# Kernel tuning notes

Hardware: AMD Instinct MI355X
Metric: run time of the kernel (lower is better)

Reference implementation:

```python
import jax, jax.numpy as jnp
import numpy as np

N = 100000      # nodes
E = 1600000     # edges (avg degree 16)
IN_DIM = 64
H = 4           # num_heads
D = 32          # out_dim per head
NEG_SLOPE = 0.1


def setup_inputs() -> dict:
    key = jax.random.key(0)
    k_x, k_src, k_dst, k_w, k_fc, k_al, k_ar = jax.random.split(key, 7)
    x = jax.random.normal(k_x, (N, IN_DIM), dtype=jnp.float32)
    src = jax.random.randint(k_src, (E,), 0, N, dtype=jnp.int32)
    dst = jax.random.randint(k_dst, (E,), 0, N, dtype=jnp.int32)
    w = jax.random.uniform(k_w, (E,), dtype=jnp.float32)
    # xavier-ish init for learned params
    W_fc = jax.random.normal(k_fc, (IN_DIM, H * D), dtype=jnp.float32) * (2.0 / (IN_DIM + H * D)) ** 0.5
    attn_l = jax.random.normal(k_al, (1, H, D), dtype=jnp.float32) * 0.1
    attn_r = jax.random.normal(k_ar, (1, H, D), dtype=jnp.float32) * 0.1
    vt = jnp.zeros((1,), dtype=jnp.float32)  # unused by forward (as in the source)
    return {"vt": vt, "x": x, "src": src, "dst": dst, "w": w,
            "W_fc": W_fc, "attn_l": attn_l, "attn_r": attn_r}


def reference(vt, x, src, dst, w, W_fc, attn_l, attn_r):
    # node projection: [N, H, D]
    feat = (x @ W_fc).reshape(-1, H, D)
    el = jnp.sum(feat * attn_l, axis=-1)  # [N, H]
    er = jnp.sum(feat * attn_r, axis=-1)  # [N, H]
    # per-edge logits: u_add_v then leaky_relu, scaled by edge weight w
    e = el[src] + er[dst]                                   # [E, H]
    e = jnp.where(e >= 0, e, NEG_SLOPE * e)                 # leaky_relu
    e = w[:, None] * e                                      # [E, H]
    # edge softmax grouped by destination node (numerically stable)
    m = jax.ops.segment_max(e, dst, num_segments=N)         # [N, H]
    ex = jnp.exp(e - m[dst])                                # [E, H]
    den = jax.ops.segment_sum(ex, dst, num_segments=N)      # [N, H]
    a = ex / den[dst]                                       # [E, H]
    # message passing: u_mul_e -> sum over incoming edges
    msg = feat[src] * a[:, :, None]                         # [E, H, D]
    out = jax.ops.segment_sum(msg, dst, num_segments=N)     # [N, H, D]
    return out
```

## Files before the change

### kernel.cpp

```cpp
#include <hip/hip_runtime.h>
#include <math.h>

#define IN_DIM 64
#define HH 4
#define CC 128
#define NEG_SLOPE 0.1f

typedef __attribute__((ext_vector_type(8))) short short8;
typedef __attribute__((ext_vector_type(4))) float f32x4;

__device__ __forceinline__ float leaky(float v) { return v >= 0.f ? v : NEG_SLOPE * v; }

__device__ __forceinline__ unsigned f2bf(float f) {
  unsigned u = __float_as_uint(f);
  unsigned r = u + 0x7FFFu + ((u >> 16) & 1u);
  return r >> 16;
}

__global__ void k_prepw(const float* __restrict__ W, unsigned* __restrict__ wt) {
  int tid = blockIdx.x * 256 + threadIdx.x;
  if (tid >= 128 * 32) return;
  int n = tid >> 5;
  int r = tid & 31;
  int b = r >> 2, h = r & 3;
  int k = b * 8 + h * 2;
  unsigned lo = f2bf(W[k * CC + n]);
  unsigned hi = f2bf(W[(k + 1) * CC + n]);
  wt[n * 32 + (b ^ (n & 7)) * 4 + h] = lo | (hi << 16);
}

__global__ __launch_bounds__(256) void k_project(
    const float* __restrict__ x, const unsigned* __restrict__ wt,
    const float* __restrict__ attn_l, const float* __restrict__ attn_r,
    unsigned char* __restrict__ featQ, float* __restrict__ scale,
    float* __restrict__ el, float* __restrict__ er, int N)
{
  __shared__ unsigned Wlds[4096];
  __shared__ float Al[CC], Ar[CC];
  int t = threadIdx.x;
  {
    const uint4* s = (const uint4*)wt;
    uint4* d = (uint4*)Wlds;
#pragma unroll
    for (int i = 0; i < 4; ++i) d[t + 256 * i] = s[t + 256 * i];
  }
  if (t < CC) { Al[t] = attn_l[t]; Ar[t] = attn_r[t]; }
  __syncthreads();

  int lane = t & 63;
  int l4 = lane >> 4, l16 = lane & 15;
  int node = blockIdx.x * 64 + (t >> 6) * 16 + l16;
  bool valid = node < N;
  int nrow = valid ? node : 0;

  short8 bfr[2];
#pragma unroll
  for (int s = 0; s < 2; ++s) {
    const float4* xp = (const float4*)&x[(size_t)nrow * 64 + s * 32 + l4 * 8];
    float4 xa = xp[0], xb = xp[1];
    union { short8 v; unsigned u[4]; } pk;
    pk.u[0] = f2bf(xa.x) | (f2bf(xa.y) << 16);
    pk.u[1] = f2bf(xa.z) | (f2bf(xa.w) << 16);
    pk.u[2] = f2bf(xb.x) | (f2bf(xb.y) << 16);
    pk.u[3] = f2bf(xb.z) | (f2bf(xb.w) << 16);
    bfr[s] = pk.v;
  }

  f32x4 acc[8];
#pragma unroll
  for (int c = 0; c < 8; ++c) acc[c] = (f32x4){0.f, 0.f, 0.f, 0.f};

#pragma unroll
  for (int c = 0; c < 8; ++c) {
    int n0 = c * 16 + l16;
    int sw = n0 & 7;
#pragma unroll
    for (int s = 0; s < 2; ++s) {
      int b = s * 4 + l4;
      union { short8 v; uint4 q; } af;
      af.q = *(const uint4*)&Wlds[n0 * 32 + (b ^ sw) * 4];
      acc[c] = __builtin_amdgcn_mfma_f32_16x16x32_bf16(af.v, bfr[s], acc[c], 0, 0, 0);
    }
  }

  float mx = 0.f;
#pragma unroll
  for (int c = 0; c < 8; ++c) {
#pragma unroll
    for (int r = 0; r < 4; ++r) mx = fmaxf(mx, fabsf(acc[c][r]));
  }
  mx = fmaxf(mx, __shfl_xor(mx, 16, 64));
  mx = fmaxf(mx, __shfl_xor(mx, 32, 64));
  float mxs = fmaxf(mx, 1e-20f);
  float inv = 127.f / mxs;

  if (valid) {
#pragma unroll
    for (int c = 0; c < 8; ++c) {
      int q0 = __float2int_rn(acc[c][0] * inv) + 128;
      int q1 = __float2int_rn(acc[c][1] * inv) + 128;
      int q2 = __float2int_rn(acc[c][2] * inv) + 128;
      int q3 = __float2int_rn(acc[c][3] * inv) + 128;
      unsigned u = (unsigned)(q0 & 0xff) | ((unsigned)(q1 & 0xff) << 8) |
                   ((unsigned)(q2 & 0xff) << 16) | ((unsigned)(q3 & 0xff) << 24);
      *(unsigned*)&featQ[(size_t)node * 128 + c * 16 + l4 * 4] = u;
    }
    if (l4 == 0) scale[node] = mxs * (1.f / 127.f);
  }

  float pl[4], pr[4];
#pragma unroll
  for (int h = 0; h < 4; ++h) {
    float sl = 0.f, sr = 0.f;
#pragma unroll
    for (int ct = 0; ct < 2; ++ct) {
      int c = 2 * h + ct;
      int cb = c * 16 + l4 * 4;
#pragma unroll
      for (int r = 0; r < 4; ++r) {
        sl = fmaf(acc[c][r], Al[cb + r], sl);
        sr = fmaf(acc[c][r], Ar[cb + r], sr);
      }
    }
    sl += __shfl_xor(sl, 16, 64); sl += __shfl_xor(sl, 32, 64);
    sr += __shfl_xor(sr, 16, 64); sr += __shfl_xor(sr, 32, 64);
    pl[h] = sl; pr[h] = sr;
  }
  if (l4 == 0 && valid) {
    *(float4*)&el[(size_t)node * 4] = make_float4(pl[0], pl[1], pl[2], pl[3]);
    *(float4*)&er[(size_t)node * 4] = make_float4(pr[0], pr[1], pr[2], pr[3]);
  }
}

__global__ __launch_bounds__(256) void k_bhist(const int* __restrict__ dst,
                                               int* __restrict__ bcnt, int E, int NB) {
  __shared__ int lh[512];
  for (int i = threadIdx.x; i < NB; i += 256) lh[i] = 0;
  __syncthreads();
  int stride = gridDim.x * 256;
  for (int i = blockIdx.x * 256 + threadIdx.x; i < E; i += stride)
    atomicAdd(&lh[dst[i] >> 8], 1);
  __syncthreads();
  for (int i = threadIdx.x; i < NB; i += 256) {
    int c = lh[i];
    if (c) atomicAdd(&bcnt[i], c);
  }
}

__global__ __launch_bounds__(512) void k_bscan(const int* __restrict__ bcnt,
                                               int* __restrict__ gbase,
                                               int* __restrict__ gcursor, int NB) {
  __shared__ int sh[512];
  int t = threadIdx.x;
  int v = (t < NB) ? bcnt[t] : 0;
  sh[t] = v;
  __syncthreads();
  for (int off = 1; off < 512; off <<= 1) {
    int a = (t >= off) ? sh[t - off] : 0;
    __syncthreads();
    sh[t] += a;
    __syncthreads();
  }
  if (t < NB) {
    int e = sh[t] - v;
    gbase[t] = e;
    gcursor[t] = e;
  }
}

__global__ __launch_bounds__(512) void k_binA(const int* __restrict__ src,
                                              const int* __restrict__ dst,
                                              const float* __restrict__ w,
                                              int* __restrict__ gcursor,
                                              uint2* __restrict__ bkt, int E, int NB) {
  __shared__ int lh[512];
  __shared__ int lbase[512];
  int t = threadIdx.x;
  for (int i = t; i < NB; i += 512) lh[i] = 0;
  __syncthreads();
  long eb = (long)blockIdx.x * 8192;
  int b[16]; int r[16]; unsigned px[16]; unsigned pw[16];
#pragma unroll
  for (int i = 0; i < 16; ++i) {
    long e = eb + t + i * 512;
    bool v = e < E;
    int d = v ? dst[e] : 0;
    b[i] = d >> 8;
    px[i] = v ? ((unsigned)src[e] | ((unsigned)(d & 255) << 20)) : 0u;
    pw[i] = v ? ((const unsigned*)w)[e] : 0u;
    r[i] = v ? atomicAdd(&lh[b[i]], 1) : -1;
  }
  __syncthreads();
  for (int i = t; i < NB; i += 512) {
    int c = lh[i];
    lbase[i] = c ? atomicAdd(&gcursor[i], c) : 0;
  }
  __syncthreads();
#pragma unroll
  for (int i = 0; i < 16; ++i)
    if (r[i] >= 0) bkt[lbase[b[i]] + r[i]] = make_uint2(px[i], pw[i]);
}

__global__ __launch_bounds__(256) void k_binB(const uint2* __restrict__ bkt,
                                              const int* __restrict__ bcnt,
                                              const int* __restrict__ gbase,
                                              int* __restrict__ offs,
                                              int2* __restrict__ sp,
                                              int N, int E, int NB) {
  __shared__ int lh[256], sc[256], lcur[256];
  int b = blockIdx.x;
  int t = threadIdx.x;
  int base_b = gbase[b];
  int cnt_b = bcnt[b];
  lh[t] = 0;
  __syncthreads();
  for (int e = t; e < cnt_b; e += 256) {
    uint2 p = bkt[base_b + e];
    atomicAdd(&lh[(p.x >> 20) & 255], 1);
  }
  __syncthreads();
  int v = lh[t];
  sc[t] = v;
  __syncthreads();
  for (int off = 1; off < 256; off <<= 1) {
    int a = (t >= off) ? sc[t - off] : 0;
    __syncthreads();
    sc[t] += a;
    __syncthreads();
  }
  int excl = sc[t] - v;
  lcur[t] = excl;
  int n0 = b << 8;
  if (n0 + t < N) offs[n0 + t] = base_b + excl;
  if (b == NB - 1 && t == 0) offs[N] = E;
  __syncthreads();
  for (int e = t; e < cnt_b; e += 256) {
    uint2 p = bkt[base_b + e];
    int d = (p.x >> 20) & 255;
    int pos = atomicAdd(&lcur[d], 1);
    sp[base_b + pos] = make_int2((int)(p.x & 0xFFFFFu), (int)p.y);
  }
}

__device__ __forceinline__ void fma16(float* acc, float& ka, float a, uint4 f) {
  ka += a;
  acc[0]  = fmaf(a, (float)( f.x        & 0xffu), acc[0]);
  acc[1]  = fmaf(a, (float)((f.x >> 8 ) & 0xffu), acc[1]);
  acc[2]  = fmaf(a, (float)((f.x >> 16) & 0xffu), acc[2]);
  acc[3]  = fmaf(a, (float)( f.x >> 24        ), acc[3]);
  acc[4]  = fmaf(a, (float)( f.y        & 0xffu), acc[4]);
  acc[5]  = fmaf(a, (float)((f.y >> 8 ) & 0xffu), acc[5]);
  acc[6]  = fmaf(a, (float)((f.y >> 16) & 0xffu), acc[6]);
  acc[7]  = fmaf(a, (float)( f.y >> 24        ), acc[7]);
  acc[8]  = fmaf(a, (float)( f.z        & 0xffu), acc[8]);
  acc[9]  = fmaf(a, (float)((f.z >> 8 ) & 0xffu), acc[9]);
  acc[10] = fmaf(a, (float)((f.z >> 16) & 0xffu), acc[10]);
  acc[11] = fmaf(a, (float)( f.z >> 24        ), acc[11]);
  acc[12] = fmaf(a, (float)( f.w        & 0xffu), acc[12]);
  acc[13] = fmaf(a, (float)((f.w >> 8 ) & 0xffu), acc[13]);
  acc[14] = fmaf(a, (float)((f.w >> 16) & 0xffu), acc[14]);
  acc[15] = fmaf(a, (float)( f.w >> 24        ), acc[15]);
}

__global__ __launch_bounds__(256) void k_aggregate(
    const int* __restrict__ offs, const int2* __restrict__ sp,
    const float* __restrict__ el, const float* __restrict__ er,
    const float* __restrict__ scale, const unsigned char* __restrict__ featQ,
    float* __restrict__ out, int N)
{
  __shared__ int    s_lds[4][64];
  __shared__ float4 a_lds[4][64];

  int t = threadIdx.x;
  int lane = t & 63, wv = t >> 6;
  int half = lane >> 5, l32 = lane & 31;
  int n = blockIdx.x * 8 + wv * 2 + half;
  if (n >= N) return;

  int off0 = offs[n], off1 = offs[n + 1];
  int deg = off1 - off0;
  int grp = l32 >> 3;
  int c8 = l32 & 7;
  int hh = c8 >> 1;
  int hlane = lane & 32;
  const unsigned char* featl = featQ + c8 * 16;
  int* slf = &s_lds[wv][half * 32];
  const float* al = (const float*)&a_lds[wv][half * 32];

  float acc[16];
#pragma unroll
  for (int i = 0; i < 16; ++i) acc[i] = 0.f;
  float ka = 0.f;

  if (deg > 0) {
    float4 erv = *reinterpret_cast<const float4*>(&er[(size_t)n * HH]);
    if (deg <= 32) {
      int dm1 = deg - 1;
      bool act = l32 < deg;
      int2 p = sp[off0 + (act ? l32 : 0)];
      int s = p.x;
      float wgt = __int_as_float(p.y);
      float sc = scale[s];

      uint4 fb[8];
#pragma unroll
      for (int k = 0; k < 4; ++k) {
        int ic = 4 * k + grp;
        int icc = ic < dm1 ? ic : dm1;
        int ss = __shfl(s, hlane + icc, 64);
        fb[k] = *reinterpret_cast<const uint4*>(featl + ((size_t)ss << 7));
      }
      if (deg > 16) {
#pragma unroll
        for (int k = 4; k < 8; ++k) {
          int ic = 4 * k + grp;
          int icc = ic < dm1 ? ic : dm1;
          int ss = __shfl(s, hlane + icc, 64);
          fb[k] = *reinterpret_cast<const uint4*>(featl + ((size_t)ss << 7));
        }
      }

      float4 elv = *reinterpret_cast<const float4*>(&el[(size_t)s * HH]);
      float x0 = act ? __expf(leaky(elv.x + erv.x) * wgt) : 0.f;
      float x1 = act ? __expf(leaky(elv.y + erv.y) * wgt) : 0.f;
      float x2 = act ? __expf(leaky(elv.z + erv.z) * wgt) : 0.f;
      float x3 = act ? __expf(leaky(elv.w + erv.w) * wgt) : 0.f;
      float d0 = x0, d1 = x1, d2 = x2, d3 = x3;
#pragma unroll
      for (int d = 16; d >= 1; d >>= 1) {
        d0 += __shfl_xor(d0, d, 64);
        d1 += __shfl_xor(d1, d, 64);
        d2 += __shfl_xor(d2, d, 64);
        d3 += __shfl_xor(d3, d, 64);
      }
      float a0 = x0 * __builtin_amdgcn_rcpf(d0) * sc;
      float a1 = x1 * __builtin_amdgcn_rcpf(d1) * sc;
      float a2 = x2 * __builtin_amdgcn_rcpf(d2) * sc;
      float a3 = x3 * __builtin_amdgcn_rcpf(d3) * sc;
      a_lds[wv][half * 32 + l32] = make_float4(a0, a1, a2, a3);

#pragma unroll
      for (int k = 0; k < 4; ++k) {
        int ic = 4 * k + grp;
        int icc = ic < dm1 ? ic : dm1;
        float a = (ic < deg) ? al[icc * 4 + hh] : 0.f;
        fma16(acc, ka, a, fb[k]);
      }
      if (deg > 16) {
#pragma unroll
        for (int k = 4; k < 8; ++k) {
          int ic = 4 * k + grp;
          int icc = ic < dm1 ? ic : dm1;
          float a = (ic < deg) ? al[icc * 4 + hh] : 0.f;
          fma16(acc, ka, a, fb[k]);
        }
      }
    } else {
      float m0 = -INFINITY, m1 = -INFINITY, m2 = -INFINITY, m3 = -INFINITY;
      for (int base = off0; base < off1; base += 32) {
        int j = base + l32;
        bool act = j < off1;
        int2 p = sp[act ? j : off0];
        float wgt = __int_as_float(p.y);
        float4 elv = *reinterpret_cast<const float4*>(&el[(size_t)p.x * HH]);
        float e0 = act ? leaky(elv.x + erv.x) * wgt : -INFINITY;
        float e1 = act ? leaky(elv.y + erv.y) * wgt : -INFINITY;
        float e2 = act ? leaky(elv.z + erv.z) * wgt : -INFINITY;
        float e3 = act ? leaky(elv.w + erv.w) * wgt : -INFINITY;
        m0 = fmaxf(m0, e0); m1 = fmaxf(m1, e1);
        m2 = fmaxf(m2, e2); m3 = fmaxf(m3, e3);
      }
#pragma unroll
      for (int d = 16; d >= 1; d >>= 1) {
        m0 = fmaxf(m0, __shfl_xor(m0, d, 64));
        m1 = fmaxf(m1, __shfl_xor(m1, d, 64));
        m2 = fmaxf(m2, __shfl_xor(m2, d, 64));
        m3 = fmaxf(m3, __shfl_xor(m3, d, 64));
      }
      float d0 = 0.f, d1 = 0.f, d2 = 0.f, d3 = 0.f;
      for (int base = off0; base < off1; base += 32) {
        int j = base + l32;
        bool act = j < off1;
        int2 p = sp[act ? j : off0];
        float wgt = __int_as_float(p.y);
        float4 elv = *reinterpret_cast<const float4*>(&el[(size_t)p.x * HH]);
        d0 += act ? __expf(leaky(elv.x + erv.x) * wgt - m0) : 0.f;
        d1 += act ? __expf(leaky(elv.y + erv.y) * wgt - m1) : 0.f;
        d2 += act ? __expf(leaky(elv.z + erv.z) * wgt - m2) : 0.f;
        d3 += act ? __expf(leaky(elv.w + erv.w) * wgt - m3) : 0.f;
      }
#pragma unroll
      for (int d = 16; d >= 1; d >>= 1) {
        d0 += __shfl_xor(d0, d, 64);
        d1 += __shfl_xor(d1, d, 64);
        d2 += __shfl_xor(d2, d, 64);
        d3 += __shfl_xor(d3, d, 64);
      }
      float i0 = __builtin_amdgcn_rcpf(d0), i1 = __builtin_amdgcn_rcpf(d1);
      float i2 = __builtin_amdgcn_rcpf(d2), i3 = __builtin_amdgcn_rcpf(d3);
      for (int base = off0; base < off1; base += 32) {
        int j = base + l32;
        bool act = j < off1;
        int2 p = sp[act ? j : off0];
        float wgt = __int_as_float(p.y);
        float sc = scale[p.x];
        float4 elv = *reinterpret_cast<const float4*>(&el[(size_t)p.x * HH]);
        float a0 = act ? __expf(leaky(elv.x + erv.x) * wgt - m0) * i0 * sc : 0.f;
        float a1 = act ? __expf(leaky(elv.y + erv.y) * wgt - m1) * i1 * sc : 0.f;
        float a2 = act ? __expf(leaky(elv.z + erv.z) * wgt - m2) * i2 * sc : 0.f;
        float a3 = act ? __expf(leaky(elv.w + erv.w) * wgt - m3) * i3 * sc : 0.f;
        slf[l32] = p.x << 7;
        a_lds[wv][half * 32 + l32] = make_float4(a0, a1, a2, a3);
        int cnt = off1 - base; if (cnt > 32) cnt = 32;
        int ne2 = (cnt + 3) >> 2;
        for (int b0 = 0; b0 < ne2; b0 += 4) {
          uint4 fb[4];
          float av[4];
#pragma unroll
          for (int k = 0; k < 4; ++k) {
            int idx = 4 * (b0 + k) + grp;
            bool vv = idx < cnt;
            int ic = vv ? idx : 0;
            av[k] = vv ? al[ic * 4 + hh] : 0.f;
            fb[k] = *reinterpret_cast<const uint4*>(featl + slf[ic]);
          }
#pragma unroll
          for (int k = 0; k < 4; ++k) fma16(acc, ka, av[k], fb[k]);
        }
      }
    }
  }
#pragma unroll
  for (int d = 8; d <= 16; d <<= 1) {
#pragma unroll
    for (int i = 0; i < 16; ++i) acc[i] += __shfl_xor(acc[i], d, 64);
    ka += __shfl_xor(ka, d, 64);
  }
  if (grp == 0) {
    float base = 128.f * ka;
    float* orow = &out[(size_t)n * CC + c8 * 16];
#pragma unroll
    for (int k = 0; k < 4; ++k) {
      f32x4 o = {acc[4 * k] - base, acc[4 * k + 1] - base,
                 acc[4 * k + 2] - base, acc[4 * k + 3] - base};
      *reinterpret_cast<f32x4*>(orow + 4 * k) = o;
    }
  }
}

extern "C" void kernel_launch(void* const* d_in, const int* in_sizes, int n_in,
                              void* d_out, int out_size, void* d_ws, size_t ws_size,
                              hipStream_t stream)
{
  const float* x      = (const float*)d_in[1];
  const int*   src    = (const int*)d_in[2];
  const int*   dst    = (const int*)d_in[3];
  const float* w      = (const float*)d_in[4];
  const float* W_fc   = (const float*)d_in[5];
  const float* attn_l = (const float*)d_in[6];
  const float* attn_r = (const float*)d_in[7];
  float* out = (float*)d_out;

  int N = in_sizes[1] / IN_DIM;
  int E = in_sizes[2];
  int NB = (N + 255) / 256;

  char* p = (char*)d_ws;
  auto alloc = [&](size_t bytes) {
    char* r = p;
    p += (bytes + 255) & ~size_t(255);
    return r;
  };
  unsigned char* featQ = (unsigned char*)alloc((size_t)N * 128);
  float* scale = (float*)alloc((size_t)N * 4);
  float* el    = (float*)alloc((size_t)N * HH * 4);
  float* er    = (float*)alloc((size_t)N * HH * 4);
  int*   offs  = (int*)alloc((size_t)(N + 1) * 4);
  int*   bcnt  = (int*)alloc(512 * 4);
  int*   gbase = (int*)alloc(512 * 4);
  int*   gcur  = (int*)alloc(512 * 4);
  unsigned* wtswz = (unsigned*)alloc(4096 * 4);
  uint2* bkt   = (uint2*)alloc((size_t)E * 8);
  int2*  sp    = (int2*)alloc((size_t)E * 8);

  hipMemsetAsync(bcnt, 0, 512 * 4, stream);

  k_prepw<<<16, 256, 0, stream>>>(W_fc, wtswz);
  k_project<<<(N + 63) / 64, 256, 0, stream>>>(x, wtswz, attn_l, attn_r,
                                               featQ, scale, el, er, N);
  k_bhist<<<256, 256, 0, stream>>>(dst, bcnt, E, NB);
  k_bscan<<<1, 512, 0, stream>>>(bcnt, gbase, gcur, NB);
  k_binA<<<(E + 8191) / 8192, 512, 0, stream>>>(src, dst, w, gcur, bkt, E, NB);
  k_binB<<<NB, 256, 0, stream>>>(bkt, bcnt, gbase, offs, sp, N, E, NB);
  k_aggregate<<<(N + 7) / 8, 256, 0, stream>>>(offs, sp, el, er, scale, featQ, out, N);
}
```

Baseline: 134.2 us.

## Fuse second-level binning with aggregation and fold weight prep into projection

Merges the per-bucket local sort (binB) into the aggregation kernel, so each block sorts its 128-node bucket's edges into shared memory and aggregates them directly. Edges no longer make a global round trip through the sorted array, except when a bucket overflows the shared capacity. Buckets shrink from 256 to 128 nodes to fit in LDS. The weight bf16 swizzle moves inside k_project, removing a launch but repeating that conversion in every block. The aggregation grid drops from about 12.5K blocks to about 782, with each block looping over 16 node pairs, which reduces parallelism and latency hiding.

```diff
diff --git a/kernel.cpp b/kernel.cpp
--- a/kernel.cpp
+++ b/kernel.cpp
@@ -5,6 +5,7 @@
 #define HH 4
 #define CC 128
 #define NEG_SLOPE 0.1f
+#define CAP 4096
 
 typedef __attribute__((ext_vector_type(8))) short short8;
 typedef __attribute__((ext_vector_type(4))) float f32x4;
@@ -17,20 +18,8 @@
   return r >> 16;
 }
 
-__global__ void k_prepw(const float* __restrict__ W, unsigned* __restrict__ wt) {
-  int tid = blockIdx.x * 256 + threadIdx.x;
-  if (tid >= 128 * 32) return;
-  int n = tid >> 5;
-  int r = tid & 31;
-  int b = r >> 2, h = r & 3;
-  int k = b * 8 + h * 2;
-  unsigned lo = f2bf(W[k * CC + n]);
-  unsigned hi = f2bf(W[(k + 1) * CC + n]);
-  wt[n * 32 + (b ^ (n & 7)) * 4 + h] = lo | (hi << 16);
-}
-
 __global__ __launch_bounds__(256) void k_project(
-    const float* __restrict__ x, const unsigned* __restrict__ wt,
+    const float* __restrict__ x, const float* __restrict__ W,
     const float* __restrict__ attn_l, const float* __restrict__ attn_r,
     unsigned char* __restrict__ featQ, float* __restrict__ scale,
     float* __restrict__ el, float* __restrict__ er, int N)
@@ -38,11 +27,15 @@
   __shared__ unsigned Wlds[4096];
   __shared__ float Al[CC], Ar[CC];
   int t = threadIdx.x;
-  {
-    const uint4* s = (const uint4*)wt;
-    uint4* d = (uint4*)Wlds;
-#pragma unroll
-    for (int i = 0; i < 4; ++i) d[t + 256 * i] = s[t + 256 * i];
+#pragma unroll
+  for (int i = 0; i < 16; ++i) {
+    int idx = t + 256 * i;
+    int nn = idx >> 5, r = idx & 31;
+    int bb = r >> 2, h2 = r & 3;
+    int kk = bb * 8 + h2 * 2;
+    unsigned lo = f2bf(W[kk * CC + nn]);
+    unsigned hi = f2bf(W[(kk + 1) * CC + nn]);
+    Wlds[nn * 32 + (bb ^ (nn & 7)) * 4 + h2] = lo | (hi << 16);
   }
   if (t < CC) { Al[t] = attn_l[t]; Ar[t] = attn_r[t]; }
   __syncthreads();
@@ -134,12 +127,12 @@
 
 __global__ __launch_bounds__(256) void k_bhist(const int* __restrict__ dst,
                                                int* __restrict__ bcnt, int E, int NB) {
-  __shared__ int lh[512];
+  __shared__ int lh[1024];
   for (int i = threadIdx.x; i < NB; i += 256) lh[i] = 0;
   __syncthreads();
   int stride = gridDim.x * 256;
   for (int i = blockIdx.x * 256 + threadIdx.x; i < E; i += stride)
-    atomicAdd(&lh[dst[i] >> 8], 1);
+    atomicAdd(&lh[dst[i] >> 7], 1);
   __syncthreads();
   for (int i = threadIdx.x; i < NB; i += 256) {
     int c = lh[i];
@@ -152,8 +145,11 @@
                                                int* __restrict__ gcursor, int NB) {
   __shared__ int sh[512];
   int t = threadIdx.x;
-  int v = (t < NB) ? bcnt[t] : 0;
-  sh[t] = v;
+  int i0 = 2 * t, i1 = 2 * t + 1;
+  int v0 = (i0 < NB) ? bcnt[i0] : 0;
+  int v1 = (i1 < NB) ? bcnt[i1] : 0;
+  int s = v0 + v1;
+  sh[t] = s;
   __syncthreads();
   for (int off = 1; off < 512; off <<= 1) {
     int a = (t >= off) ? sh[t - off] : 0;
@@ -161,11 +157,9 @@
     sh[t] += a;
     __syncthreads();
   }
-  if (t < NB) {
-    int e = sh[t] - v;
-    gbase[t] = e;
-    gcursor[t] = e;
-  }
+  int e = sh[t] - s;
+  if (i0 < NB) { gbase[i0] = e;       gcursor[i0] = e; }
+  if (i1 < NB) { gbase[i1] = e + v0;  gcursor[i1] = e + v0; }
 }
 
 __global__ __launch_bounds__(512) void k_binA(const int* __restrict__ src,
@@ -173,8 +167,8 @@
                                               const float* __restrict__ w,
                                               int* __restrict__ gcursor,
                                               uint2* __restrict__ bkt, int E, int NB) {
-  __shared__ int lh[512];
-  __shared__ int lbase[512];
+  __shared__ int lh[1024];
+  __shared__ int lbase[1024];
   int t = threadIdx.x;
   for (int i = t; i < NB; i += 512) lh[i] = 0;
   __syncthreads();
@@ -185,8 +179,8 @@
     long e = eb + t + i * 512;
     bool v = e < E;
     int d = v ? dst[e] : 0;
-    b[i] = d >> 8;
-    px[i] = v ? ((unsigned)src[e] | ((unsigned)(d & 255) << 20)) : 0u;
+    b[i] = d >> 7;
+    px[i] = v ? ((unsigned)src[e] | ((unsigned)(d & 127) << 20)) : 0u;
     pw[i] = v ? ((const unsigned*)w)[e] : 0u;
     r[i] = v ? atomicAdd(&lh[b[i]], 1) : -1;
   }
@@ -199,47 +193,6 @@
 #pragma unroll
   for (int i = 0; i < 16; ++i)
     if (r[i] >= 0) bkt[lbase[b[i]] + r[i]] = make_uint2(px[i], pw[i]);
-}
-
-__global__ __launch_bounds__(256) void k_binB(const uint2* __restrict__ bkt,
-                                              const int* __restrict__ bcnt,
-                                              const int* __restrict__ gbase,
-                                              int* __restrict__ offs,
-                                              int2* __restrict__ sp,
-                                              int N, int E, int NB) {
-  __shared__ int lh[256], sc[256], lcur[256];
-  int b = blockIdx.x;
-  int t = threadIdx.x;
-  int base_b = gbase[b];
-  int cnt_b = bcnt[b];
-  lh[t] = 0;
-  __syncthreads();
-  for (int e = t; e < cnt_b; e += 256) {
-    uint2 p = bkt[base_b + e];
-    atomicAdd(&lh[(p.x >> 20) & 255], 1);
-  }
-  __syncthreads();
-  int v = lh[t];
-  sc[t] = v;
-  __syncthreads();
-  for (int off = 1; off < 256; off <<= 1) {
-    int a = (t >= off) ? sc[t - off] : 0;
-    __syncthreads();
-    sc[t] += a;
-    __syncthreads();
-  }
-  int excl = sc[t] - v;
-  lcur[t] = excl;
-  int n0 = b << 8;
-  if (n0 + t < N) offs[n0 + t] = base_b + excl;
-  if (b == NB - 1 && t == 0) offs[N] = E;
-  __syncthreads();
-  for (int e = t; e < cnt_b; e += 256) {
-    uint2 p = bkt[base_b + e];
-    int d = (p.x >> 20) & 255;
-    int pos = atomicAdd(&lcur[d], 1);
-    sp[base_b + pos] = make_int2((int)(p.x & 0xFFFFFu), (int)p.y);
-  }
 }
 
 __device__ __forceinline__ void fma16(float* acc, float& ka, float a, uint4 f) {
@@ -262,23 +215,60 @@
   acc[15] = fmaf(a, (float)( f.w >> 24        ), acc[15]);
 }
 
-__global__ __launch_bounds__(256) void k_aggregate(
-    const int* __restrict__ offs, const int2* __restrict__ sp,
+__global__ __launch_bounds__(256) void k_binagg(
+    const uint2* __restrict__ bkt, const int* __restrict__ bcnt,
+    const int* __restrict__ gbase,
     const float* __restrict__ el, const float* __restrict__ er,
     const float* __restrict__ scale, const unsigned char* __restrict__ featQ,
-    float* __restrict__ out, int N)
+    int2* __restrict__ spg, float* __restrict__ out, int N)
 {
+  __shared__ int  loffs[129];
+  __shared__ int  lh[128], lcur[128];
+  __shared__ int2 spl[CAP];
   __shared__ int    s_lds[4][64];
   __shared__ float4 a_lds[4][64];
 
+  int b = blockIdx.x;
   int t = threadIdx.x;
+  int base_b = gbase[b];
+  int cnt_b = bcnt[b];
+  bool ovf = cnt_b > CAP;
+
+  if (t < 128) lh[t] = 0;
+  __syncthreads();
+  for (int e = t; e < cnt_b; e += 256) {
+    uint2 p = bkt[base_b + e];
+    atomicAdd(&lh[(p.x >> 20) & 127], 1);
+  }
+  __syncthreads();
+  if (t < 128) lcur[t] = lh[t];
+  __syncthreads();
+  for (int off = 1; off < 128; off <<= 1) {
+    int a = (t < 128 && t >= off) ? lcur[t - off] : 0;
+    __syncthreads();
+    if (t < 128) lcur[t] += a;
+    __syncthreads();
+  }
+  if (t < 128) {
+    loffs[t + 1] = lcur[t];
+    if (t == 0) loffs[0] = 0;
+  }
+  __syncthreads();
+  if (t < 128) lcur[t] = loffs[t];
+  __syncthreads();
+  for (int e = t; e < cnt_b; e += 256) {
+    uint2 p = bkt[base_b + e];
+    int d = (p.x >> 20) & 127;
+    int pos = atomicAdd(&lcur[d], 1);
+    int2 v = make_int2((int)(p.x & 0xFFFFFu), (int)p.y);
+    if (!ovf) spl[pos] = v; else spg[base_b + pos] = v;
+  }
+  __syncthreads();
+
+  const int2* sps = ovf ? (spg + base_b) : (const int2*)spl;
+
   int lane = t & 63, wv = t >> 6;
   int half = lane >> 5, l32 = lane & 31;
-  int n = blockIdx.x * 8 + wv * 2 + half;
-  if (n >= N) return;
-
-  int off0 = offs[n], off1 = offs[n + 1];
-  int deg = off1 - off0;
   int grp = l32 >> 3;
   int c8 = l32 & 7;
   int hh = c8 >> 1;
@@ -287,163 +277,171 @@
   int* slf = &s_lds[wv][half * 32];
   const float* al = (const float*)&a_lds[wv][half * 32];
 
-  float acc[16];
-#pragma unroll
-  for (int i = 0; i < 16; ++i) acc[i] = 0.f;
-  float ka = 0.f;
-
-  if (deg > 0) {
-    float4 erv = *reinterpret_cast<const float4*>(&er[(size_t)n * HH]);
-    if (deg <= 32) {
-      int dm1 = deg - 1;
-      bool act = l32 < deg;
-      int2 p = sp[off0 + (act ? l32 : 0)];
-      int s = p.x;
-      float wgt = __int_as_float(p.y);
-      float sc = scale[s];
-
-      uint4 fb[8];
-#pragma unroll
-      for (int k = 0; k < 4; ++k) {
-        int ic = 4 * k + grp;
-        int icc = ic < dm1 ? ic : dm1;
-        int ss = __shfl(s, hlane + icc, 64);
-        fb[k] = *reinterpret_cast<const uint4*>(featl + ((size_t)ss << 7));
-      }
-      if (deg > 16) {
-#pragma unroll
-        for (int k = 4; k < 8; ++k) {
+  for (int it = 0; it < 16; ++it) {
+    int ln = it * 8 + wv * 2 + half;
+    int n = (b << 7) + ln;
+    if (n >= N) continue;
+    int off0 = loffs[ln], off1 = loffs[ln + 1];
+    int deg = off1 - off0;
+
+    float acc[16];
+#pragma unroll
+    for (int i = 0; i < 16; ++i) acc[i] = 0.f;
+    float ka = 0.f;
+
+    if (deg > 0) {
+      float4 erv = *reinterpret_cast<const float4*>(&er[(size_t)n * HH]);
+      if (deg <= 32) {
+        int dm1 = deg - 1;
+        bool act = l32 < deg;
+        int2 p = sps[off0 + (act ? l32 : 0)];
+        int s = p.x;
+        float wgt = __int_as_float(p.y);
+        float sc = scale[s];
+
+        uint4 fb[8];
+#pragma unroll
+        for (int k = 0; k < 4; ++k) {
           int ic = 4 * k + grp;
           int icc = ic < dm1 ? ic : dm1;
           int ss = __shfl(s, hlane + icc, 64);
           fb[k] = *reinterpret_cast<const uint4*>(featl + ((size_t)ss << 7));
         }
-      }
-
-      float4 elv = *reinterpret_cast<const float4*>(&el[(size_t)s * HH]);
-      float x0 = act ? __expf(leaky(elv.x + erv.x) * wgt) : 0.f;
-      float x1 = act ? __expf(leaky(elv.y + erv.y) * wgt) : 0.f;
-      float x2 = act ? __expf(leaky(elv.z + erv.z) * wgt) : 0.f;
-      float x3 = act ? __expf(leaky(elv.w + erv.w) * wgt) : 0.f;
-      float d0 = x0, d1 = x1, d2 = x2, d3 = x3;
-#pragma unroll
-      for (int d = 16; d >= 1; d >>= 1) {
-        d0 += __shfl_xor(d0, d, 64);
-        d1 += __shfl_xor(d1, d, 64);
-        d2 += __shfl_xor(d2, d, 64);
-        d3 += __shfl_xor(d3, d, 64);
-      }
-      float a0 = x0 * __builtin_amdgcn_rcpf(d0) * sc;
-      float a1 = x1 * __builtin_amdgcn_rcpf(d1) * sc;
-      float a2 = x2 * __builtin_amdgcn_rcpf(d2) * sc;
-      float a3 = x3 * __builtin_amdgcn_rcpf(d3) * sc;
-      a_lds[wv][half * 32 + l32] = make_float4(a0, a1, a2, a3);
-
-#pragma unroll
-      for (int k = 0; k < 4; ++k) {
-        int ic = 4 * k + grp;
-        int icc = ic < dm1 ? ic : dm1;
-        float a = (ic < deg) ? al[icc * 4 + hh] : 0.f;
-        fma16(acc, ka, a, fb[k]);
-      }
-      if (deg > 16) {
-#pragma unroll
-        for (int k = 4; k < 8; ++k) {
+        if (deg > 16) {
+#pragma unroll
+          for (int k = 4; k < 8; ++k) {
+            int ic = 4 * k + grp;
+            int icc = ic < dm1 ? ic : dm1;
+            int ss = __shfl(s, hlane + icc, 64);
+            fb[k] = *reinterpret_cast<const uint4*>(featl + ((size_t)ss << 7));
+          }
+        }
+
+        float4 elv = *reinterpret_cast<const float4*>(&el[(size_t)s * HH]);
+        float x0 = act ? __expf(leaky(elv.x + erv.x) * wgt) : 0.f;
+        float x1 = act ? __expf(leaky(elv.y + erv.y) * wgt) : 0.f;
+        float x2 = act ? __expf(leaky(elv.z + erv.z) * wgt) : 0.f;
+        float x3 = act ? __expf(leaky(elv.w + erv.w) * wgt) : 0.f;
+        float d0 = x0, d1 = x1, d2 = x2, d3 = x3;
+#pragma unroll
+        for (int d = 16; d >= 1; d >>= 1) {
+          d0 += __shfl_xor(d0, d, 64);
+          d1 += __shfl_xor(d1, d, 64);
+          d2 += __shfl_xor(d2, d, 64);
+          d3 += __shfl_xor(d3, d, 64);
+        }
+        float a0 = x0 * __builtin_amdgcn_rcpf(d0) * sc;
+        float a1 = x1 * __builtin_amdgcn_rcpf(d1) * sc;
+        float a2 = x2 * __builtin_amdgcn_rcpf(d2) * sc;
+        float a3 = x3 * __builtin_amdgcn_rcpf(d3) * sc;
+        a_lds[wv][half * 32 + l32] = make_float4(a0, a1, a2, a3);
+
+#pragma unroll
+        for (int k = 0; k < 4; ++k) {
           int ic = 4 * k + grp;
           int icc = ic < dm1 ? ic : dm1;
           float a = (ic < deg) ? al[icc * 4 + hh] : 0.f;
           fma16(acc, ka, a, fb[k]);
         }
+        if (deg > 16) {
+#pragma unroll
+          for (int k = 4; k < 8; ++k) {
+            int ic = 4 * k + grp;
+            int icc = ic < dm1 ? ic : dm1;
+            float a = (ic < deg) ? al[icc * 4 + hh] : 0.f;
+            fma16(acc, ka, a, fb[k]);
+          }
+        }
+      } else {
+        float m0 = -INFINITY, m1 = -INFINITY, m2 = -INFINITY, m3 = -INFINITY;
+        for (int base = off0; base < off1; base += 32) {
+          int j = base + l32;
+          bool act = j < off1;
+          int2 p = sps[act ? j : off0];
+          float wgt = __int_as_float(p.y);
+          float4 elv = *reinterpret_cast<const float4*>(&el[(size_t)p.x * HH]);
+          float e0 = act ? leaky(elv.x + erv.x) * wgt : -INFINITY;
+          float e1 = act ? leaky(elv.y + erv.y) * wgt : -INFINITY;
+          float e2 = act ? leaky(elv.z + erv.z) * wgt : -INFINITY;
+          float e3 = act ? leaky(elv.w + erv.w) * wgt : -INFINITY;
+          m0 = fmaxf(m0, e0); m1 = fmaxf(m1, e1);
+          m2 = fmaxf(m2, e2); m3 = fmaxf(m3, e3);
+        }
+#pragma unroll
+        for (int d = 16; d >= 1; d >>= 1) {
+          m0 = fmaxf(m0, __shfl_xor(m0, d, 64));
+          m1 = fmaxf(m1, __shfl_xor(m1, d, 64));
+          m2 = fmaxf(m2, __shfl_xor(m2, d, 64));
+          m3 = fmaxf(m3, __shfl_xor(m3, d, 64));
+        }
+        float d0 = 0.f, d1 = 0.f, d2 = 0.f, d3 = 0.f;
+        for (int base = off0; base < off1; base += 32) {
+          int j = base + l32;
+          bool act = j < off1;
+          int2 p = sps[act ? j : off0];
+          float wgt = __int_as_float(p.y);
+          float4 elv = *reinterpret_cast<const float4*>(&el[(size_t)p.x * HH]);
+          d0 += act ? __expf(leaky(elv.x + erv.x) * wgt - m0) : 0.f;
+          d1 += act ? __expf(leaky(elv.y + erv.y) * wgt - m1) : 0.f;
+          d2 += act ? __expf(leaky(elv.z + erv.z) * wgt - m2) : 0.f;
+          d3 += act ? __expf(leaky(elv.w + erv.w) * wgt - m3) : 0.f;
+        }
+#pragma unroll
+        for (int d = 16; d >= 1; d >>= 1) {
+          d0 += __shfl_xor(d0, d, 64);
+          d1 += __shfl_xor(d1, d, 64);
+          d2 += __shfl_xor(d2, d, 64);
+          d3 += __shfl_xor(d3, d, 64);
+        }
+        float i0 = __builtin_amdgcn_rcpf(d0), i1 = __builtin_amdgcn_rcpf(d1);
+        float i2 = __builtin_amdgcn_rcpf(d2), i3 = __builtin_amdgcn_rcpf(d3);
+        for (int base = off0; base < off1; base += 32) {
+          int j = base + l32;
+          bool act = j < off1;
+          int2 p = sps[act ? j : off0];
+          float wgt = __int_as_float(p.y);
+          float sc = scale[p.x];
+          float4 elv = *reinterpret_cast<const float4*>(&el[(size_t)p.x * HH]);
+          float a0 = act ? __expf(leaky(elv.x + erv.x) * wgt - m0) * i0 * sc : 0.f;
+          float a1 = act ? __expf(leaky(elv.y + erv.y) * wgt - m1) * i1 * sc : 0.f;
+          float a2 = act ? __expf(leaky(elv.z + erv.z) * wgt - m2) * i2 * sc : 0.f;
+          float a3 = act ? __expf(leaky(elv.w + erv.w) * wgt - m3) * i3 * sc : 0.f;
+          slf[l32] = p.x << 7;
+          a_lds[wv][half * 32 + l32] = make_float4(a0, a1, a2, a3);
+          int cnt = off1 - base; if (cnt > 32) cnt = 32;
+          int ne2 = (cnt + 3) >> 2;
+          for (int b0 = 0; b0 < ne2; b0 += 4) {
+            uint4 fb[4];
+            float av[4];
+#pragma unroll
+            for (int k = 0; k < 4; ++k) {
+              int idx = 4 * (b0 + k) + grp;
+              bool vv = idx < cnt;
+              int ic = vv ? idx : 0;
+              av[k] = vv ? al[ic * 4 + hh] : 0.f;
+              fb[k] = *reinterpret_cast<const uint4*>(featl + slf[ic]);
+            }
+#pragma unroll
+            for (int k = 0; k < 4; ++k) fma16(acc, ka, av[k], fb[k]);
+          }
+        }
       }
-    } else {
-      float m0 = -INFINITY, m1 = -INFINITY, m2 = -INFINITY, m3 = -INFINITY;
-      for (int base = off0; base < off1; base += 32) {
-        int j = base + l32;
-        bool act = j < off1;
-        int2 p = sp[act ? j : off0];
-        float wgt = __int_as_float(p.y);
-        float4 elv = *reinterpret_cast<const float4*>(&el[(size_t)p.x * HH]);
-        float e0 = act ? leaky(elv.x + erv.x) * wgt : -INFINITY;
-        float e1 = act ? leaky(elv.y + erv.y) * wgt : -INFINITY;
-        float e2 = act ? leaky(elv.z + erv.z) * wgt : -INFINITY;
-        float e3 = act ? leaky(elv.w + erv.w) * wgt : -INFINITY;
-        m0 = fmaxf(m0, e0); m1 = fmaxf(m1, e1);
-        m2 = fmaxf(m2, e2); m3 = fmaxf(m3, e3);
+    }
+#pragma unroll
+    for (int d = 8; d <= 16; d <<= 1) {
+#pragma unroll
+      for (int i = 0; i < 16; ++i) acc[i] += __shfl_xor(acc[i], d, 64);
+      ka += __shfl_xor(ka, d, 64);
+    }
+    if (grp == 0) {
+      float base = 128.f * ka;
+      float* orow = &out[(size_t)n * CC + c8 * 16];
+#pragma unroll
+      for (int k = 0; k < 4; ++k) {
+        f32x4 o = {acc[4 * k] - base, acc[4 * k + 1] - base,
+                   acc[4 * k + 2] - base, acc[4 * k + 3] - base};
+        *reinterpret_cast<f32x4*>(orow + 4 * k) = o;
       }
-#pragma unroll
-      for (int d = 16; d >= 1; d >>= 1) {
-        m0 = fmaxf(m0, __shfl_xor(m0, d, 64));
-        m1 = fmaxf(m1, __shfl_xor(m1, d, 64));
-        m2 = fmaxf(m2, __shfl_xor(m2, d, 64));
-        m3 = fmaxf(m3, __shfl_xor(m3, d, 64));
-      }
-      float d0 = 0.f, d1 = 0.f, d2 = 0.f, d3 = 0.f;
-      for (int base = off0; base < off1; base += 32) {
-        int j = base + l32;
-        bool act = j < off1;
-        int2 p = sp[act ? j : off0];
-        float wgt = __int_as_float(p.y);
-        float4 elv = *reinterpret_cast<const float4*>(&el[(size_t)p.x * HH]);
-        d0 += act ? __expf(leaky(elv.x + erv.x) * wgt - m0) : 0.f;
-        d1 += act ? __expf(leaky(elv.y + erv.y) * wgt - m1) : 0.f;
-        d2 += act ? __expf(leaky(elv.z + erv.z) * wgt - m2) : 0.f;
-        d3 += act ? __expf(leaky(elv.w + erv.w) * wgt - m3) : 0.f;
-      }
-#pragma unroll
-      for (int d = 16; d >= 1; d >>= 1) {
-        d0 += __shfl_xor(d0, d, 64);
-        d1 += __shfl_xor(d1, d, 64);
-        d2 += __shfl_xor(d2, d, 64);
-        d3 += __shfl_xor(d3, d, 64);
-      }
-      float i0 = __builtin_amdgcn_rcpf(d0), i1 = __builtin_amdgcn_rcpf(d1);
-      float i2 = __builtin_amdgcn_rcpf(d2), i3 = __builtin_amdgcn_rcpf(d3);
-      for (int base = off0; base < off1; base += 32) {
-        int j = base + l32;
-        bool act = j < off1;
-        int2 p = sp[act ? j : off0];
-        float wgt = __int_as_float(p.y);
-        float sc = scale[p.x];
-        float4 elv = *reinterpret_cast<const float4*>(&el[(size_t)p.x * HH]);
-        float a0 = act ? __expf(leaky(elv.x + erv.x) * wgt - m0) * i0 * sc : 0.f;
-        float a1 = act ? __expf(leaky(elv.y + erv.y) * wgt - m1) * i1 * sc : 0.f;
-        float a2 = act ? __expf(leaky(elv.z + erv.z) * wgt - m2) * i2 * sc : 0.f;
-        float a3 = act ? __expf(leaky(elv.w + erv.w) * wgt - m3) * i3 * sc : 0.f;
-        slf[l32] = p.x << 7;
-        a_lds[wv][half * 32 + l32] = make_float4(a0, a1, a2, a3);
-        int cnt = off1 - base; if (cnt > 32) cnt = 32;
-        int ne2 = (cnt + 3) >> 2;
-        for (int b0 = 0; b0 < ne2; b0 += 4) {
-          uint4 fb[4];
-          float av[4];
-#pragma unroll
-          for (int k = 0; k < 4; ++k) {
-            int idx = 4 * (b0 + k) + grp;
-            bool vv = idx < cnt;
-            int ic = vv ? idx : 0;
-            av[k] = vv ? al[ic * 4 + hh] : 0.f;
-            fb[k] = *reinterpret_cast<const uint4*>(featl + slf[ic]);
-          }
-#pragma unroll
-          for (int k = 0; k < 4; ++k) fma16(acc, ka, av[k], fb[k]);
-        }
-      }
-    }
-  }
-#pragma unroll
-  for (int d = 8; d <= 16; d <<= 1) {
-#pragma unroll
-    for (int i = 0; i < 16; ++i) acc[i] += __shfl_xor(acc[i], d, 64);
-    ka += __shfl_xor(ka, d, 64);
-  }
-  if (grp == 0) {
-    float base = 128.f * ka;
-    float* orow = &out[(size_t)n * CC + c8 * 16];
-#pragma unroll
-    for (int k = 0; k < 4; ++k) {
-      f32x4 o = {acc[4 * k] - base, acc[4 * k + 1] - base,
-                 acc[4 * k + 2] - base, acc[4 * k + 3] - base};
-      *reinterpret_cast<f32x4*>(orow + 4 * k) = o;
     }
   }
 }
@@ -463,7 +461,7 @@
 
   int N = in_sizes[1] / IN_DIM;
   int E = in_sizes[2];
-  int NB = (N + 255) / 256;
+  int NB = (N + 127) / 128;
 
   char* p = (char*)d_ws;
   auto alloc = [&](size_t bytes) {
@@ -475,22 +473,19 @@
   float* scale = (float*)alloc((size_t)N * 4);
   float* el    = (float*)alloc((size_t)N * HH * 4);
   float* er    = (float*)alloc((size_t)N * HH * 4);
-  int*   offs  = (int*)alloc((size_t)(N + 1) * 4);
-  int*   bcnt  = (int*)alloc(512 * 4);
-  int*   gbase = (int*)alloc(512 * 4);
-  int*   gcur  = (int*)alloc(512 * 4);
-  unsigned* wtswz = (unsigned*)alloc(4096 * 4);
+  int*   bcnt  = (int*)alloc(1024 * 4);
+  int*   gbase = (int*)alloc(1024 * 4);
+  int*   gcur  = (int*)alloc(1024 * 4);
   uint2* bkt   = (uint2*)alloc((size_t)E * 8);
-  int2*  sp    = (int2*)alloc((size_t)E * 8);
-
-  hipMemsetAsync(bcnt, 0, 512 * 4, stream);
-
-  k_prepw<<<16, 256, 0, stream>>>(W_fc, wtswz);
-  k_project<<<(N + 63) / 64, 256, 0, stream>>>(x, wtswz, attn_l, attn_r,
+  int2*  spg   = (int2*)alloc((size_t)E * 8);
+
+  hipMemsetAsync(bcnt, 0, 1024 * 4, stream);
+
+  k_project<<<(N + 63) / 64, 256, 0, stream>>>(x, W_fc, attn_l, attn_r,
                                                featQ, scale, el, er, N);
   k_bhist<<<256, 256, 0, stream>>>(dst, bcnt, E, NB);
   k_bscan<<<1, 512, 0, stream>>>(bcnt, gbase, gcur, NB);
   k_binA<<<(E + 8191) / 8192, 512, 0, stream>>>(src, dst, w, gcur, bkt, E, NB);
-  k_binB<<<NB, 256, 0, stream>>>(bkt, bcnt, gbase, offs, sp, N, E, NB);
-  k_aggregate<<<(N + 7) / 8, 256, 0, stream>>>(offs, sp, el, er, scale, featQ, out, N);
-}
+  k_binagg<<<NB, 256, 0, stream>>>(bkt, bcnt, gbase, el, er, scale, featQ,
+                                   spg, out, N);
+}
```

Result: slower. 170.2 us (+26.8%).
